# Performance work log

Hardware: AMD Instinct MI355X
Metric: run time of the kernel (lower is better)

Reference implementation:

```python
import jax, jax.numpy as jnp
import numpy as np

B, S, D, H = 4, 2048, 1024, 16
HD = D // H
NEG = -1e30


def setup_inputs() -> dict:
    key = jax.random.key(0)
    ks = jax.random.split(key, 6)
    scale = 1.0 / np.sqrt(D)
    return {
        "q": jax.random.normal(ks[0], (B, S, D), jnp.float32),
        "k": jax.random.normal(ks[1], (B, S, D), jnp.float32),
        "v": jax.random.normal(ks[2], (B, S, D), jnp.float32),
        "mask": jnp.ones((B, 1, S), jnp.float32),
        "wq": jax.random.normal(ks[3], (D, D), jnp.float32) * scale,
        "bq": jnp.zeros((D,), jnp.float32),
        "wk": jax.random.normal(ks[4], (D, D), jnp.float32) * scale,
        "bk": jnp.zeros((D,), jnp.float32),
        "wv": jax.random.normal(ks[5], (D, D), jnp.float32) * scale,
        "bv": jnp.zeros((D,), jnp.float32),
    }


def _heads(x):
    # (B,S,D) -> (B,H,S,HD)
    return x.reshape(B, S, H, HD).transpose(0, 2, 1, 3)


def reference(q, k, v, mask, wq, bq, wk, bk, wv, bv):
    # pointwise Conv1D(kernel=1) == linear: x @ W^T + b (W: (out,in))
    qh = _heads(jnp.einsum('bsd,ed->bse', q, wq) + bq)
    kh = _heads(jnp.einsum('bsd,ed->bse', k, wk) + bk)
    vh = _heads(jnp.einsum('bsd,ed->bse', v, wv) + bv)
    scores = jnp.einsum('bhqd,bhkd->bhqk', qh, kh) / jnp.sqrt(jnp.float32(HD))
    # mask_logits: x + (1 - mask) * -1e30, mask (B,1,S) -> (B,1,1,S)
    scores = scores + (1.0 - mask[:, None, :, :]) * NEG
    probs = jax.nn.softmax(scores, axis=-1)  # dropout is identity in eval
    ctx = jnp.einsum('bhqk,bhkd->bhqd', probs, vh)
    return ctx.transpose(0, 2, 1, 3).reshape(B, S, D)
```

## Files before the change

kernel.cpp:

```cpp
#include <hip/hip_runtime.h>
#include <math.h>

typedef __attribute__((ext_vector_type(8)))  _Float16 f16x8;
typedef __attribute__((ext_vector_type(4)))  _Float16 f16x4;
typedef __attribute__((ext_vector_type(2)))  __fp16   h16x2;
typedef __attribute__((ext_vector_type(4)))  float    f32x4;
typedef __attribute__((ext_vector_type(16))) float    f32x16;
typedef unsigned int u32;

static constexpr int B  = 4;
static constexpr int S  = 2048;
static constexpr int D  = 1024;
static constexpr int H  = 16;
static constexpr int HD = 64;

union U64cvt { f16x4 h; ushort4 u; };
union W4 { u32 w[4]; f16x8 v; };

__device__ __forceinline__ void gld16(const void* g, void* l) {
    __builtin_amdgcn_global_load_lds((const u32*)g, (u32*)l, 16, 0, 0);
}

__device__ __forceinline__ void cvtwr16(const float4& x, const float4& y, void* dst) {
    W4 w;
    w.w[0] = __builtin_bit_cast(u32, __builtin_amdgcn_cvt_pkrtz(x.x, x.y));
    w.w[1] = __builtin_bit_cast(u32, __builtin_amdgcn_cvt_pkrtz(x.z, x.w));
    w.w[2] = __builtin_bit_cast(u32, __builtin_amdgcn_cvt_pkrtz(y.x, y.y));
    w.w[3] = __builtin_bit_cast(u32, __builtin_amdgcn_cvt_pkrtz(y.z, y.w));
    *(f16x8*)dst = w.v;
}

__global__ __launch_bounds__(256)
void proj_qkv(const float* __restrict__ qi, const float* __restrict__ ki,
              const float* __restrict__ vi,
              const float* __restrict__ wqp, const float* __restrict__ wkp,
              const float* __restrict__ wvp,
              const float* __restrict__ bqp, const float* __restrict__ bkp,
              const float* __restrict__ bvp,
              unsigned short* __restrict__ ws)
{
    const int bid = blockIdx.x;
    const int xcd = bid & 7;
    const int idx = bid >> 3;
    const int z   = idx / 64;
    const int r2  = idx - z * 64;
    const int mpl = r2 >> 3;
    const int np  = r2 & 7;
    const int mp  = (xcd >> 1) * 16 + (xcd & 1) * 8 + mpl;
    const int m0  = mp * 128;
    const int n0  = np * 128;

    const float* A    = (z == 0) ? qi  : (z == 1) ? ki  : vi;
    const float* W    = (z == 0) ? wqp : (z == 1) ? wkp : wvp;
    const float* bias = (z == 0) ? bqp : (z == 1) ? bkp : bvp;
    unsigned short* out = ws + (size_t)z * ((size_t)B * S * D);

    const int tid  = threadIdx.x;
    const int lane = tid & 63;
    const int wid  = tid >> 6;
    const int wr   = wid >> 1;
    const int wc   = wid & 1;

    __shared__ __align__(16) unsigned char lA[2][8192];
    __shared__ __align__(16) unsigned char lB[2][8192];

    f32x4 acc[4][4];
#pragma unroll
    for (int i = 0; i < 4; ++i)
#pragma unroll
        for (int j = 0; j < 4; ++j) acc[i][j] = (f32x4){0.f, 0.f, 0.f, 0.f};

    const int rb = (lane >> 4) * 16;

    int srow[2], sc8[2], soff[2];
#pragma unroll
    for (int i = 0; i < 2; ++i) {
        const int f = tid + 256 * i;
        srow[i] = f >> 2;
        sc8[i]  = f & 3;
        soff[i] = ((f >> 2) * 64 + (f & 3) * 16) ^ ((((f >> 2)) & 7) << 4);
    }

#pragma unroll
    for (int i = 0; i < 2; ++i) {
        const float* pa = A + (size_t)(m0 + srow[i]) * D + sc8[i] * 8;
        const float* pw = W + (size_t)(n0 + srow[i]) * D + sc8[i] * 8;
        cvtwr16(*(const float4*)pa, *(const float4*)(pa + 4), lA[0] + soff[i]);
        cvtwr16(*(const float4*)pw, *(const float4*)(pw + 4), lB[0] + soff[i]);
    }
    float4 pa0[2], pa1[2], pw0[2], pw1[2];
#pragma unroll
    for (int i = 0; i < 2; ++i) {
        const float* pa = A + (size_t)(m0 + srow[i]) * D + 32 + sc8[i] * 8;
        const float* pw = W + (size_t)(n0 + srow[i]) * D + 32 + sc8[i] * 8;
        pa0[i] = *(const float4*)pa;  pa1[i] = *(const float4*)(pa + 4);
        pw0[i] = *(const float4*)pw;  pw1[i] = *(const float4*)(pw + 4);
    }
    __syncthreads();

    for (int kt = 0; kt < 32; ++kt) {
        const int cb = kt & 1, nx = cb ^ 1;

        if (kt < 31) {
#pragma unroll
            for (int i = 0; i < 2; ++i) {
                cvtwr16(pa0[i], pa1[i], lA[nx] + soff[i]);
                cvtwr16(pw0[i], pw1[i], lB[nx] + soff[i]);
            }
        }

        f16x8 af[4], bf[4];
#pragma unroll
        for (int mi = 0; mi < 4; ++mi) {
            const int row = wr * 64 + mi * 16 + (lane & 15);
            af[mi] = *(const f16x8*)(lA[cb] + ((row * 64 + rb) ^ ((row & 7) << 4)));
        }
#pragma unroll
        for (int ni = 0; ni < 4; ++ni) {
            const int row = wc * 64 + ni * 16 + (lane & 15);
            bf[ni] = *(const f16x8*)(lB[cb] + ((row * 64 + rb) ^ ((row & 7) << 4)));
        }

        if (kt < 30) {
            const int k2 = (kt + 2) * 32;
#pragma unroll
            for (int i = 0; i < 2; ++i) {
                const float* pa = A + (size_t)(m0 + srow[i]) * D + k2 + sc8[i] * 8;
                const float* pw = W + (size_t)(n0 + srow[i]) * D + k2 + sc8[i] * 8;
                pa0[i] = *(const float4*)pa;  pa1[i] = *(const float4*)(pa + 4);
                pw0[i] = *(const float4*)pw;  pw1[i] = *(const float4*)(pw + 4);
            }
        }

        __builtin_amdgcn_s_setprio(1);
#pragma unroll
        for (int mi = 0; mi < 4; ++mi)
#pragma unroll
            for (int ni = 0; ni < 4; ++ni)
                acc[mi][ni] = __builtin_amdgcn_mfma_f32_16x16x32_f16(af[mi], bf[ni], acc[mi][ni], 0, 0, 0);
        __builtin_amdgcn_s_setprio(0);

        __syncthreads();
    }

#pragma unroll
    for (int mi = 0; mi < 4; ++mi) {
        const int gmBase = m0 + wr * 64 + mi * 16 + ((lane >> 4) << 2);
        const int b  = gmBase >> 11;
        const int s0 = gmBase & 2047;
        const int tV   = s0 >> 6;
        const int kv6  = s0 & 63;
        const int ksg  = kv6 >> 4;
        const int hi2v = (kv6 >> 3) & 1;
        const int jb   = kv6 & 7;
#pragma unroll
        for (int ni = 0; ni < 4; ++ni) {
            const int gn = n0 + wc * 64 + ni * 16 + (lane & 15);
            const float bb = bias[gn];
            const int hh = gn >> 6;
            const int hd = gn & 63;
            const size_t bhbase = ((size_t)b * H + hh) * ((size_t)S * HD);
            if (z == 0) {
#pragma unroll
                for (int r = 0; r < 4; ++r) {
                    const int gm = gmBase + r;
                    const _Float16 hv = (_Float16)(acc[mi][ni][r] + bb);
                    out[bhbase + (size_t)(gm & 2047) * HD + hd] =
                        __builtin_bit_cast(unsigned short, hv);
                }
            } else if (z == 1) {
                const int ks   = hd >> 4;
                const int hi2k = (hd >> 3) & 1;
                const int j    = hd & 7;
#pragma unroll
                for (int r = 0; r < 4; ++r) {
                    const int s = (gmBase + r) & 2047;
                    const int t = s >> 6;
                    const int q = ((s >> 5) & 1) * 4 + ks;
                    const _Float16 hv = (_Float16)(acc[mi][ni][r] + bb);
                    out[bhbase + (((size_t)t * 8 + q) * 64 + hi2k * 32 + (s & 31)) * 8 + j] =
                        __builtin_bit_cast(unsigned short, hv);
                }
            } else {
                const int nb  = hd >> 5;
                const int c31 = hd & 31;
                const int q   = nb * 4 + ksg;
                U64cvt uu;
#pragma unroll
                for (int r = 0; r < 4; ++r)
                    uu.h[r] = (_Float16)(acc[mi][ni][r] + bb);
                *(ushort4*)(out + bhbase +
                    (((size_t)tV * 8 + q) * 64 + hi2v * 32 + c31) * 8 + jb) = uu.u;
            }
        }
    }
}

__global__ __launch_bounds__(256)
void attn_f16(const unsigned short* __restrict__ qh,
              const unsigned short* __restrict__ kf,
              const unsigned short* __restrict__ vf,
              const float* __restrict__ mask,
              float* __restrict__ out)
{
    const int flat = blockIdx.y * gridDim.x + blockIdx.x;
    const int sw   = (flat & 7) * 128 + (flat >> 3);
    const int bh   = sw >> 4;
    const int q0   = (sw & 15) * 128;

    const int b = bh >> 4;
    const int h = bh & 15;
    const unsigned short* Q  = qh + (size_t)bh * S * HD;
    const unsigned short* KF = kf + (size_t)bh * S * HD;
    const unsigned short* VF = vf + (size_t)bh * S * HD;

    const int tid  = threadIdx.x;
    const int lane = tid & 63;
    const int wid  = tid >> 6;
    const int l31  = lane & 31;
    const int hi2  = lane >> 5;

    __shared__ __align__(16) unsigned char Kl[2][8192];
    __shared__ __align__(16) unsigned char Vl[2][8192];
    __shared__ __align__(16) float maskb[2][64];

    const int ldsA = wid * 1024;
    const int ldsB = wid * 1024 + 4096;
    const int g0   = tid * 8;
    const int g1   = tid * 8 + 2048;

    const float C = 0.18033688011112042f;
    const float SHIFT = -5.770780163555854f;

    f16x8 aq[4];
    {
        const unsigned short* qrow = Q + (size_t)(q0 + wid * 32 + l31) * HD;
#pragma unroll
        for (int ks = 0; ks < 4; ++ks)
            aq[ks] = *(const f16x8*)(qrow + ks * 16 + hi2 * 8);
    }

    float ls0 = 0.f, ls1 = 0.f;
    f32x16 accO[2];
    accO[0] = (f32x16){};
    accO[1] = (f32x16){};
    const h16x2 one2 = {(__fp16)1.0f, (__fp16)1.0f};

    gld16(KF + g0, Kl[0] + ldsA);
    gld16(KF + g1, Kl[0] + ldsB);
    gld16(VF + g0, Vl[0] + ldsA);
    gld16(VF + g1, Vl[0] + ldsB);
    if (tid < 64)
        maskb[0][tid] = fmaf(1.0f - mask[(size_t)b * S + tid], -1.4426950408889634e30f, SHIFT);
    __syncthreads();

    const int lane16 = lane * 16;
    for (int t = 0; t < S / 64; ++t) {
        const int cb = t & 1, nx = cb ^ 1;
        const unsigned char* Kc = Kl[cb];
        const unsigned char* Vc = Vl[cb];

        if (t < S / 64 - 1) {
            const int nt = (t + 1) * 4096;
            gld16(KF + nt + g0, Kl[nx] + ldsA);
            gld16(KF + nt + g1, Kl[nx] + ldsB);
            gld16(VF + nt + g0, Vl[nx] + ldsA);
            gld16(VF + nt + g1, Vl[nx] + ldsB);
            if (tid < 64)
                maskb[nx][tid] = fmaf(1.0f - mask[(size_t)b * S + (t + 1) * 64 + tid],
                                      -1.4426950408889634e30f, SHIFT);
        }

        f32x16 p[2];
        p[0] = (f32x16){};
        p[1] = (f32x16){};
        __builtin_amdgcn_s_setprio(1);
#pragma unroll
        for (int kb = 0; kb < 2; ++kb)
#pragma unroll
            for (int ks = 0; ks < 4; ++ks) {
                const f16x8 ak = *(const f16x8*)(Kc + lane16 + (kb * 4 + ks) * 1024);
                p[kb] = __builtin_amdgcn_mfma_f32_32x32x16_f16(ak, aq[ks], p[kb], 0, 0, 0);
            }
        __builtin_amdgcn_s_setprio(0);

        f16x8 pa[4];
#pragma unroll
        for (int kb = 0; kb < 2; ++kb) {
            float pe[16];
#pragma unroll
            for (int g = 0; g < 4; ++g) {
                const f32x4 mg = *(const f32x4*)(&maskb[cb][kb * 32 + g * 8 + hi2 * 4]);
#pragma unroll
                for (int e = 0; e < 4; ++e)
                    pe[g * 4 + e] = exp2f(fmaf(p[kb][g * 4 + e], C, mg[e]));
            }
#pragma unroll
            for (int ks2 = 0; ks2 < 2; ++ks2) {
                const int o = ks2 * 8;
                const h16x2 h0 = __builtin_amdgcn_cvt_pkrtz(pe[o + 0], pe[o + 1]);
                const h16x2 h1 = __builtin_amdgcn_cvt_pkrtz(pe[o + 2], pe[o + 3]);
                const h16x2 h2 = __builtin_amdgcn_cvt_pkrtz(pe[o + 4], pe[o + 5]);
                const h16x2 h3 = __builtin_amdgcn_cvt_pkrtz(pe[o + 6], pe[o + 7]);
                ls0 = __builtin_amdgcn_fdot2(h0, one2, ls0, false);
                ls1 = __builtin_amdgcn_fdot2(h1, one2, ls1, false);
                ls0 = __builtin_amdgcn_fdot2(h2, one2, ls0, false);
                ls1 = __builtin_amdgcn_fdot2(h3, one2, ls1, false);
                u32 a0 = __builtin_bit_cast(u32, h0);
                u32 a1 = __builtin_bit_cast(u32, h1);
                u32 a2 = __builtin_bit_cast(u32, h2);
                u32 a3 = __builtin_bit_cast(u32, h3);
                asm volatile("v_permlane32_swap_b32 %0, %1" : "+v"(a0), "+v"(a2));
                asm volatile("v_permlane32_swap_b32 %0, %1" : "+v"(a1), "+v"(a3));
                W4 w;
                w.w[0] = a0; w.w[1] = a1; w.w[2] = a2; w.w[3] = a3;
                pa[kb * 2 + ks2] = w.v;
            }
        }

        __builtin_amdgcn_s_setprio(1);
#pragma unroll
        for (int nb = 0; nb < 2; ++nb)
#pragma unroll
            for (int ksg = 0; ksg < 4; ++ksg) {
                const f16x8 bv = *(const f16x8*)(Vc + lane16 + (nb * 4 + ksg) * 1024);
                accO[nb] = __builtin_amdgcn_mfma_f32_32x32x16_f16(pa[ksg], bv, accO[nb], 0, 0, 0);
            }
        __builtin_amdgcn_s_setprio(0);

        __syncthreads();
    }

    float lsum = ls0 + ls1;
    lsum += __shfl_xor(lsum, 32);
    const float linv = 1.0f / lsum;

    float lr[16];
#pragma unroll
    for (int r = 0; r < 16; ++r)
        lr[r] = __shfl(linv, (r & 3) + 8 * (r >> 2) + 4 * hi2);

#pragma unroll
    for (int nb = 0; nb < 2; ++nb) {
        const int dcol = h * HD + nb * 32 + l31;
#pragma unroll
        for (int r = 0; r < 16; ++r) {
            const int qrow = q0 + wid * 32 + (r & 3) + 8 * (r >> 2) + 4 * hi2;
            out[((size_t)b * S + qrow) * D + dcol] = accO[nb][r] * lr[r];
        }
    }
}

extern "C" void kernel_launch(void* const* d_in, const int* in_sizes, int n_in,
                              void* d_out, int out_size, void* d_ws, size_t ws_size,
                              hipStream_t stream)
{
    const float* q    = (const float*)d_in[0];
    const float* k    = (const float*)d_in[1];
    const float* v    = (const float*)d_in[2];
    const float* mask = (const float*)d_in[3];
    const float* wq   = (const float*)d_in[4];
    const float* bq   = (const float*)d_in[5];
    const float* wk   = (const float*)d_in[6];
    const float* bk   = (const float*)d_in[7];
    const float* wv   = (const float*)d_in[8];
    const float* bv   = (const float*)d_in[9];

    unsigned short* ws = (unsigned short*)d_ws;
    const size_t per = (size_t)B * S * D;

    proj_qkv<<<1536, 256, 0, stream>>>(q, k, v, wq, wk, wv, bq, bk, bv, ws);

    dim3 ga(S / 128, B * H);
    attn_f16<<<ga, 256, 0, stream>>>(ws, ws + per, ws + 2 * per, mask, (float*)d_out);
}
```

Measured before the change: 227.5 us.

## Pre-convert inputs to fp16, use async LDS loads in projection, MFMA row sums

Adds a separate pass that converts the q/k/v activations and weights to fp16 in workspace. A new projection GEMM then streams those fp16 tiles straight into LDS with global_load_lds, using a rotated-column swizzle in place of the register-staged fp32 load and convert. In the attention kernel, the per-row softmax denominator now comes from an extra MFMA against a ones vector rather than fdot2 accumulations and shuffles. This costs an extra full read and write pass over the inputs and needs a larger workspace; if the workspace is too small the old path runs.

Result: no change. 228.9 us (+0.6%).

```diff
diff --git a/kernel.cpp b/kernel.cpp
--- a/kernel.cpp
+++ b/kernel.cpp
@@ -28,6 +28,175 @@
     w.w[2] = __builtin_bit_cast(u32, __builtin_amdgcn_cvt_pkrtz(y.x, y.y));
     w.w[3] = __builtin_bit_cast(u32, __builtin_amdgcn_cvt_pkrtz(y.z, y.w));
     *(f16x8*)dst = w.v;
+}
+
+__global__ __launch_bounds__(256)
+void cvt_prep(const float* __restrict__ q, const float* __restrict__ k,
+              const float* __restrict__ v,
+              const float* __restrict__ wq, const float* __restrict__ wk,
+              const float* __restrict__ wv,
+              unsigned short* __restrict__ dst)
+{
+    const int c = blockIdx.x * 256 + threadIdx.x;
+    const float* src;
+    size_t idx;
+    if (c < 3145728) {
+        const int a = c >> 20;
+        src = (a == 0) ? q : (a == 1) ? k : v;
+        idx = (size_t)(c & 1048575) * 8;
+    } else {
+        const int c2 = c - 3145728;
+        const int a = c2 >> 17;
+        src = (a == 0) ? wq : (a == 1) ? wk : wv;
+        idx = (size_t)(c2 & 131071) * 8;
+    }
+    const float4 x = *(const float4*)(src + idx);
+    const float4 y = *(const float4*)(src + idx + 4);
+    cvtwr16(x, y, dst + (size_t)c * 8);
+}
+
+__global__ __launch_bounds__(256)
+void proj_f16(const unsigned short* __restrict__ af16,
+              const unsigned short* __restrict__ wf16,
+              const float* __restrict__ bqp, const float* __restrict__ bkp,
+              const float* __restrict__ bvp,
+              unsigned short* __restrict__ outs)
+{
+    const int bid = blockIdx.x;
+    const int xcd = bid & 7;
+    const int idx = bid >> 3;
+    const int z   = idx / 64;
+    const int r2  = idx - z * 64;
+    const int mpl = r2 >> 3;
+    const int np  = r2 & 7;
+    const int mp  = (xcd >> 1) * 16 + (xcd & 1) * 8 + mpl;
+    const int m0  = mp * 128;
+    const int n0  = np * 128;
+
+    const unsigned short* A  = af16 + (size_t)z * 8388608;
+    const unsigned short* Wf = wf16 + (size_t)z * 1048576;
+    const float* bias = (z == 0) ? bqp : (z == 1) ? bkp : bvp;
+    unsigned short* out = outs + (size_t)z * 8388608;
+
+    const int tid  = threadIdx.x;
+    const int lane = tid & 63;
+    const int wid  = tid >> 6;
+    const int wr   = wid >> 1;
+    const int wc   = wid & 1;
+
+    __shared__ __align__(16) unsigned char lA[2][8192];
+    __shared__ __align__(16) unsigned char lB[2][8192];
+
+    f32x4 acc[4][4];
+#pragma unroll
+    for (int i = 0; i < 4; ++i)
+#pragma unroll
+        for (int j = 0; j < 4; ++j) acc[i][j] = (f32x4){0.f, 0.f, 0.f, 0.f};
+
+    int grow[2], gcol[2], lbase[2];
+#pragma unroll
+    for (int i = 0; i < 2; ++i) {
+        const int c = tid + 256 * i;
+        grow[i]  = c >> 2;
+        gcol[i]  = ((c & 3) - (grow[i] >> 1)) & 3;
+        lbase[i] = (c & ~63) * 16;
+    }
+
+#pragma unroll
+    for (int i = 0; i < 2; ++i) {
+        gld16(A  + (size_t)(m0 + grow[i]) * D + gcol[i] * 8, lA[0] + lbase[i]);
+        gld16(Wf + (size_t)(n0 + grow[i]) * D + gcol[i] * 8, lB[0] + lbase[i]);
+    }
+    __syncthreads();
+
+    for (int kt = 0; kt < 32; ++kt) {
+        const int cb = kt & 1, nx = cb ^ 1;
+
+        if (kt < 31) {
+            const int k1 = (kt + 1) * 32;
+#pragma unroll
+            for (int i = 0; i < 2; ++i) {
+                gld16(A  + (size_t)(m0 + grow[i]) * D + k1 + gcol[i] * 8, lA[nx] + lbase[i]);
+                gld16(Wf + (size_t)(n0 + grow[i]) * D + k1 + gcol[i] * 8, lB[nx] + lbase[i]);
+            }
+        }
+
+        f16x8 af[4], bf[4];
+#pragma unroll
+        for (int mi = 0; mi < 4; ++mi) {
+            const int row = wr * 64 + mi * 16 + (lane & 15);
+            const int cc  = ((lane >> 4) + (row >> 1)) & 3;
+            af[mi] = *(const f16x8*)(lA[cb] + row * 64 + cc * 16);
+        }
+#pragma unroll
+        for (int ni = 0; ni < 4; ++ni) {
+            const int row = wc * 64 + ni * 16 + (lane & 15);
+            const int cc  = ((lane >> 4) + (row >> 1)) & 3;
+            bf[ni] = *(const f16x8*)(lB[cb] + row * 64 + cc * 16);
+        }
+
+        __builtin_amdgcn_s_setprio(1);
+#pragma unroll
+        for (int mi = 0; mi < 4; ++mi)
+#pragma unroll
+            for (int ni = 0; ni < 4; ++ni)
+                acc[mi][ni] = __builtin_amdgcn_mfma_f32_16x16x32_f16(af[mi], bf[ni], acc[mi][ni], 0, 0, 0);
+        __builtin_amdgcn_s_setprio(0);
+
+        __syncthreads();
+    }
+
+#pragma unroll
+    for (int mi = 0; mi < 4; ++mi) {
+        const int gmBase = m0 + wr * 64 + mi * 16 + ((lane >> 4) << 2);
+        const int b  = gmBase >> 11;
+        const int s0 = gmBase & 2047;
+        const int tV   = s0 >> 6;
+        const int kv6  = s0 & 63;
+        const int ksg  = kv6 >> 4;
+        const int hi2v = (kv6 >> 3) & 1;
+        const int jb   = kv6 & 7;
+#pragma unroll
+        for (int ni = 0; ni < 4; ++ni) {
+            const int gn = n0 + wc * 64 + ni * 16 + (lane & 15);
+            const float bb = bias[gn];
+            const int hh = gn >> 6;
+            const int hd = gn & 63;
+            const size_t bhbase = ((size_t)b * H + hh) * ((size_t)S * HD);
+            if (z == 0) {
+#pragma unroll
+                for (int r = 0; r < 4; ++r) {
+                    const int gm = gmBase + r;
+                    const _Float16 hv = (_Float16)(acc[mi][ni][r] + bb);
+                    out[bhbase + (size_t)(gm & 2047) * HD + hd] =
+                        __builtin_bit_cast(unsigned short, hv);
+                }
+            } else if (z == 1) {
+                const int ks   = hd >> 4;
+                const int hi2k = (hd >> 3) & 1;
+                const int j    = hd & 7;
+#pragma unroll
+                for (int r = 0; r < 4; ++r) {
+                    const int s = (gmBase + r) & 2047;
+                    const int t = s >> 6;
+                    const int q = ((s >> 5) & 1) * 4 + ks;
+                    const _Float16 hv = (_Float16)(acc[mi][ni][r] + bb);
+                    out[bhbase + (((size_t)t * 8 + q) * 64 + hi2k * 32 + (s & 31)) * 8 + j] =
+                        __builtin_bit_cast(unsigned short, hv);
+                }
+            } else {
+                const int nb  = hd >> 5;
+                const int c31 = hd & 31;
+                const int q   = nb * 4 + ksg;
+                U64cvt uu;
+#pragma unroll
+                for (int r = 0; r < 4; ++r)
+                    uu.h[r] = (_Float16)(acc[mi][ni][r] + bb);
+                *(ushort4*)(out + bhbase +
+                    (((size_t)tV * 8 + q) * 64 + hi2v * 32 + c31) * 8 + jb) = uu.u;
+            }
+        }
+    }
 }
 
 __global__ __launch_bounds__(256)
@@ -100,7 +269,6 @@
 
     for (int kt = 0; kt < 32; ++kt) {
         const int cb = kt & 1, nx = cb ^ 1;
-
         if (kt < 31) {
 #pragma unroll
             for (int i = 0; i < 2; ++i) {
@@ -108,7 +276,6 @@
                 cvtwr16(pw0[i], pw1[i], lB[nx] + soff[i]);
             }
         }
-
         f16x8 af[4], bf[4];
 #pragma unroll
         for (int mi = 0; mi < 4; ++mi) {
@@ -120,7 +287,6 @@
             const int row = wc * 64 + ni * 16 + (lane & 15);
             bf[ni] = *(const f16x8*)(lB[cb] + ((row * 64 + rb) ^ ((row & 7) << 4)));
         }
-
         if (kt < 30) {
             const int k2 = (kt + 2) * 32;
 #pragma unroll
@@ -131,7 +297,6 @@
                 pw0[i] = *(const float4*)pw;  pw1[i] = *(const float4*)(pw + 4);
             }
         }
-
         __builtin_amdgcn_s_setprio(1);
 #pragma unroll
         for (int mi = 0; mi < 4; ++mi)
@@ -139,7 +304,6 @@
             for (int ni = 0; ni < 4; ++ni)
                 acc[mi][ni] = __builtin_amdgcn_mfma_f32_16x16x32_f16(af[mi], bf[ni], acc[mi][ni], 0, 0, 0);
         __builtin_amdgcn_s_setprio(0);
-
         __syncthreads();
     }
 
@@ -240,11 +404,12 @@
             aq[ks] = *(const f16x8*)(qrow + ks * 16 + hi2 * 8);
     }
 
-    float ls0 = 0.f, ls1 = 0.f;
-    f32x16 accO[2];
+    f32x16 accO[2], accL;
     accO[0] = (f32x16){};
     accO[1] = (f32x16){};
-    const h16x2 one2 = {(__fp16)1.0f, (__fp16)1.0f};
+    accL    = (f32x16){};
+    const f16x8 onesv = {(_Float16)1.f, (_Float16)1.f, (_Float16)1.f, (_Float16)1.f,
+                         (_Float16)1.f, (_Float16)1.f, (_Float16)1.f, (_Float16)1.f};
 
     gld16(KF + g0, Kl[0] + ldsA);
     gld16(KF + g1, Kl[0] + ldsB);
@@ -298,18 +463,10 @@
 #pragma unroll
             for (int ks2 = 0; ks2 < 2; ++ks2) {
                 const int o = ks2 * 8;
-                const h16x2 h0 = __builtin_amdgcn_cvt_pkrtz(pe[o + 0], pe[o + 1]);
-                const h16x2 h1 = __builtin_amdgcn_cvt_pkrtz(pe[o + 2], pe[o + 3]);
-                const h16x2 h2 = __builtin_amdgcn_cvt_pkrtz(pe[o + 4], pe[o + 5]);
-                const h16x2 h3 = __builtin_amdgcn_cvt_pkrtz(pe[o + 6], pe[o + 7]);
-                ls0 = __builtin_amdgcn_fdot2(h0, one2, ls0, false);
-                ls1 = __builtin_amdgcn_fdot2(h1, one2, ls1, false);
-                ls0 = __builtin_amdgcn_fdot2(h2, one2, ls0, false);
-                ls1 = __builtin_amdgcn_fdot2(h3, one2, ls1, false);
-                u32 a0 = __builtin_bit_cast(u32, h0);
-                u32 a1 = __builtin_bit_cast(u32, h1);
-                u32 a2 = __builtin_bit_cast(u32, h2);
-                u32 a3 = __builtin_bit_cast(u32, h3);
+                u32 a0 = __builtin_bit_cast(u32, __builtin_amdgcn_cvt_pkrtz(pe[o + 0], pe[o + 1]));
+                u32 a1 = __builtin_bit_cast(u32, __builtin_amdgcn_cvt_pkrtz(pe[o + 2], pe[o + 3]));
+                u32 a2 = __builtin_bit_cast(u32, __builtin_amdgcn_cvt_pkrtz(pe[o + 4], pe[o + 5]));
+                u32 a3 = __builtin_bit_cast(u32, __builtin_amdgcn_cvt_pkrtz(pe[o + 6], pe[o + 7]));
                 asm volatile("v_permlane32_swap_b32 %0, %1" : "+v"(a0), "+v"(a2));
                 asm volatile("v_permlane32_swap_b32 %0, %1" : "+v"(a1), "+v"(a3));
                 W4 w;
@@ -326,19 +483,18 @@
                 const f16x8 bv = *(const f16x8*)(Vc + lane16 + (nb * 4 + ksg) * 1024);
                 accO[nb] = __builtin_amdgcn_mfma_f32_32x32x16_f16(pa[ksg], bv, accO[nb], 0, 0, 0);
             }
+#pragma unroll
+        for (int ksg = 0; ksg < 4; ++ksg)
+            accL = __builtin_amdgcn_mfma_f32_32x32x16_f16(pa[ksg], onesv, accL, 0, 0, 0);
         __builtin_amdgcn_s_setprio(0);
 
         __syncthreads();
     }
 
-    float lsum = ls0 + ls1;
-    lsum += __shfl_xor(lsum, 32);
-    const float linv = 1.0f / lsum;
-
     float lr[16];
 #pragma unroll
     for (int r = 0; r < 16; ++r)
-        lr[r] = __shfl(linv, (r & 3) + 8 * (r >> 2) + 4 * hi2);
+        lr[r] = 1.0f / accL[r];
 
 #pragma unroll
     for (int nb = 0; nb < 2; ++nb) {
@@ -367,10 +523,20 @@
     const float* bv   = (const float*)d_in[9];
 
     unsigned short* ws = (unsigned short*)d_ws;
-    const size_t per = (size_t)B * S * D;
-
-    proj_qkv<<<1536, 256, 0, stream>>>(q, k, v, wq, wk, wv, bq, bk, bv, ws);
+    const size_t per  = (size_t)B * S * D;
+    const size_t wsz  = 1048576;
+    const size_t need = (3 * per + 3 * wsz + 3 * per) * 2;
 
     dim3 ga(S / 128, B * H);
-    attn_f16<<<ga, 256, 0, stream>>>(ws, ws + per, ws + 2 * per, mask, (float*)d_out);
-}
+    if (ws_size >= need) {
+        unsigned short* af16 = ws;
+        unsigned short* wf16 = ws + 3 * per;
+        unsigned short* outs = ws + 3 * per + 3 * wsz;
+        cvt_prep<<<13824, 256, 0, stream>>>(q, k, v, wq, wk, wv, af16);
+        proj_f16<<<1536, 256, 0, stream>>>(af16, wf16, bq, bk, bv, outs);
+        attn_f16<<<ga, 256, 0, stream>>>(outs, outs + per, outs + 2 * per, mask, (float*)d_out);
+    } else {
+        proj_qkv<<<1536, 256, 0, stream>>>(q, k, v, wq, wk, wv, bq, bk, bv, ws);
+        attn_f16<<<ga, 256, 0, stream>>>(ws, ws + per, ws + 2 * per, mask, (float*)d_out);
+    }
+}
```
